# Performance work log

Measured on AMD Instinct MI355X. Metric: run time of the kernel, lower is better.

The kernel has to match this reference:

```python
import jax, jax.numpy as jnp
import numpy as np

DIM = 256
HEADS = 8
P = 8   # patch_size
S = 4   # stride


def _pos_index(p):
    # Swin-style relative position index, computed statically in numpy
    coord = np.arange(p)
    ii, jj = np.meshgrid(coord, coord, indexing='ij')
    cf = np.stack([ii.ravel(), jj.ravel()])              # [2, p*p]
    rel = cf[:, :, None] - cf[:, None, :]                # [2, P, P]
    rel = rel.transpose(1, 2, 0).copy()                  # [P, P, 2]
    rel[:, :, 0] += p - 1
    rel[:, :, 1] += p - 1
    rel[:, :, 0] *= 2 * p - 1
    return jnp.asarray(rel.sum(-1))                      # [P, P] int


def setup_inputs() -> dict:
    key = jax.random.key(0)
    k1, k2, k3, k4, k5 = jax.random.split(key, 5)
    x = jax.random.normal(k1, (2, DIM, 96, 96), jnp.float32)
    # depthwise 1x1 conv on 3*dim channels -> per-channel scale + bias
    qkv_w = jax.random.normal(k2, (3 * DIM,), jnp.float32) * 0.1 + 1.0
    qkv_b = jax.random.normal(k3, (3 * DIM,), jnp.float32) * 0.1
    # 1x1 conv dim->dim, no bias
    out_w = jax.random.normal(k4, (DIM, DIM), jnp.float32) * 0.05
    # relative position bias table, trunc_normal(std=0.02)
    pos_table = jax.random.normal(k5, ((2 * P - 1) ** 2, HEADS), jnp.float32) * 0.02
    return {"x": x, "qkv_w": qkv_w, "qkv_b": qkv_b, "out_w": out_w, "pos_table": pos_table}


def reference(x, qkv_w, qkv_b, out_w, pos_table):
    B, C, H, W = x.shape
    h, p, s = HEADS, P, S
    d = C // h
    pad = p - s
    # replicate pad right/bottom
    xp = jnp.pad(x, ((0, 0), (0, 0), (0, pad), (0, pad)), mode='edge')
    x3 = jnp.concatenate([xp, xp, xp], axis=1)           # [B, 3C, Hp, Wp]
    # depthwise 1x1 conv == per-channel affine
    qkv = x3 * qkv_w[None, :, None, None] + qkv_b[None, :, None, None]
    n = (H + pad - p) // s + 1                           # patches per side
    idx = (jnp.arange(n) * s)[:, None] + jnp.arange(p)[None, :]   # [n, p]
    # unfold: extract overlapping p x p patches with stride s
    t = qkv[:, :, idx, :]                                # [B, 3C, n, p, Wp]
    t = t[:, :, :, :, idx]                               # [B, 3C, n, p, n, p]
    t = t.transpose(0, 1, 2, 4, 3, 5)                    # [B, 3C, n, n, p, p]
    t = t.reshape(B, 3, h, d, n * n, p * p).transpose(1, 0, 2, 4, 5, 3)  # [3,B,h,N,P,d]
    q, k, v = t[0] * (d ** -0.5), t[1], t[2]
    bias = pos_table[_pos_index(p)]                      # [P, P, h]
    bias = bias.transpose(2, 0, 1)                       # [h, P, P]
    attn = jnp.einsum('bhnqd,bhnkd->bhnqk', q, k) + bias[None, :, None]
    attn = jax.nn.softmax(attn, axis=-1)
    out = jnp.einsum('bhnqk,bhnkd->bhnqd', attn, v)      # [B, h, N, P, d]
    # keep only the top-left stride x stride of each patch, then fold (non-overlap)
    out = out.reshape(B, h, n, n, p, p, d)[:, :, :, :, :s, :s]   # [B,h,n,n,s,s,d]
    out = out.transpose(0, 1, 6, 2, 4, 3, 5).reshape(B, C, H, W)
    return jnp.einsum('oc,bchw->bohw', out_w, out)
```

## Files before the change

### kernel.cpp

```cpp
#include <hip/hip_runtime.h>

typedef float f4 __attribute__((ext_vector_type(4)));
typedef float f32x4 __attribute__((ext_vector_type(4)));
typedef __bf16 bf16x8 __attribute__((ext_vector_type(8)));
typedef __bf16 bf16x4 __attribute__((ext_vector_type(4)));

#define NPSIDE 24

#define XS(ch_, r_, c_) xs[(ch_) * 169 + (r_) * 21 + (c_)]

__global__ __launch_bounds__(256, 4) void patch_attn(
    const float* __restrict__ x,
    const float* __restrict__ qkv_w,
    const float* __restrict__ qkv_b,
    const float* __restrict__ pos_table,
    const float* __restrict__ wmat,
    __bf16* __restrict__ mid,
    __bf16* __restrict__ wbf)
{
    __shared__ float xs[32 * 169];
    __shared__ __bf16 Ps[4][16][72];

    const int t = threadIdx.x;

    if (blockIdx.x < 64) {
        const int i = (blockIdx.x * 256 + t) * 4;
        const int o = i >> 8, c = i & 255;
        const f4 v = *(const f4*)&wmat[i];
        bf16x4 ov;
        #pragma unroll
        for (int j = 0; j < 4; ++j) ov[j] = (__bf16)v[j];
        *(bf16x4*)&wbf[((o >> 4) * 8 + (c >> 5)) * 512 + (o & 15) * 32 + (c & 31)] = ov;
    }

    const int raw = blockIdx.x;
    const int xcd = raw & 7;
    const int idx = raw >> 3;
    const int bs  = xcd * 36 + (idx >> 3);
    const int head = idx & 7;
    const int b   = bs / 144;
    const int r   = bs % 144;
    const int ni   = r / 6;
    const int nj0p = (r % 6) * 4;
    const int c0   = head * 32;

    #pragma unroll
    for (int i = 0; i < 5; ++i) {
        const int idx2 = i * 256 + t;
        const int ch  = idx2 / 40;
        const int rem = idx2 % 40;
        const int row = rem / 5, cg = rem % 5;
        const int rg  = min(4 * ni + row, 95);
        const int cg4 = 16 * (r % 6) + 4 * cg;
        const float* xrow = x + (((size_t)b * 256 + c0 + ch) * 96 + rg) * 96;
        f4 v;
        if (cg4 <= 92) {
            v = *(const f4*)&xrow[cg4];
        } else {
            const float s = xrow[95];
            v = (f4){s, s, s, s};
        }
        float* xdst = &XS(ch, row, 4 * cg);
        xdst[0] = v.x; xdst[1] = v.y; xdst[2] = v.z; xdst[3] = v.w;
    }

    const int wv = t >> 6, l = t & 63;
    const int l16 = l & 15, lg = l >> 4;
    const float qscale = 0.17677669529663687f;

    float kw8[8], kb8[8], qw8[8], qb8[8];
    #pragma unroll
    for (int j = 0; j < 8; ++j) {
        const int c = c0 + 8 * lg + j;
        kw8[j] = qkv_w[256 + c];
        kb8[j] = qkv_b[256 + c];
        qw8[j] = qkv_w[c] * qscale;
        qb8[j] = qkv_b[c] * qscale;
    }
    float vw2[2], vb2[2];
    #pragma unroll
    for (int nt = 0; nt < 2; ++nt) {
        const int c = c0 + nt * 16 + l16;
        vw2[nt] = qkv_w[512 + c];
        vb2[nt] = qkv_b[512 + c];
    }

    __syncthreads();

    const int nj  = nj0p + wv;
    const int cbl = 4 * wv;

    bf16x8 qf;
    {
        const int qrow = l16 >> 2, qcol = cbl + (l16 & 3);
        #pragma unroll
        for (int j = 0; j < 8; ++j)
            qf[j] = (__bf16)(XS(8 * lg + j, qrow, qcol) * qw8[j] + qb8[j]);
    }

    const f32x4 zf = {0.f, 0.f, 0.f, 0.f};
    f32x4 sacc[4];
    #pragma unroll
    for (int t4 = 0; t4 < 4; ++t4) {
        const int px = l16 + 16 * t4;
        const int kr = px >> 3, kc = cbl + (px & 7);
        bf16x8 kf;
        #pragma unroll
        for (int j = 0; j < 8; ++j)
            kf[j] = (__bf16)(XS(8 * lg + j, kr, kc) * kw8[j] + kb8[j]);
        sacc[t4] = __builtin_amdgcn_mfma_f32_16x16x32_bf16(qf, kf, zf, 0, 0, 0);
    }

    float sv[4][4], rinv[4];
    #pragma unroll
    for (int rr = 0; rr < 4; ++rr) {
        const int qrow = lg * 4 + rr;
        const int qi = qrow >> 2, qj = qrow & 3;
        float m = -1e30f;
        #pragma unroll
        for (int t4 = 0; t4 < 4; ++t4) {
            const int kcol = l16 + 16 * t4;
            const int ki = kcol >> 3, kj = kcol & 7;
            const float s = sacc[t4][rr]
                + pos_table[((qi - ki + 7) * 15 + (qj - kj + 7)) * 8 + head];
            sv[t4][rr] = s;
            m = fmaxf(m, s);
        }
        #pragma unroll
        for (int off = 8; off >= 1; off >>= 1)
            m = fmaxf(m, __shfl_xor(m, off, 16));
        float sum = 0.f;
        #pragma unroll
        for (int t4 = 0; t4 < 4; ++t4) {
            const float p = __expf(sv[t4][rr] - m);
            sv[t4][rr] = p;
            sum += p;
        }
        #pragma unroll
        for (int off = 8; off >= 1; off >>= 1)
            sum += __shfl_xor(sum, off, 16);
        rinv[rr] = 1.0f / sum;
        #pragma unroll
        for (int t4 = 0; t4 < 4; ++t4)
            Ps[wv][qrow][l16 + 16 * t4] = (__bf16)sv[t4][rr];
    }

    f32x4 oa = zf, ob = zf;
    #pragma unroll
    for (int kt = 0; kt < 2; ++kt) {
        bf16x8 pf = *(const bf16x8*)&Ps[wv][l16][lg * 8 + 32 * kt];
        bf16x8 v0, v1;
        #pragma unroll
        for (int j = 0; j < 8; ++j) {
            const int px = kt * 32 + 8 * lg + j;
            const int vr = px >> 3, vc = cbl + (px & 7);
            v0[j] = (__bf16)(XS(l16,      vr, vc) * vw2[0] + vb2[0]);
            v1[j] = (__bf16)(XS(16 + l16, vr, vc) * vw2[1] + vb2[1]);
        }
        oa = __builtin_amdgcn_mfma_f32_16x16x32_bf16(pf, v0, oa, 0, 0, 0);
        ob = __builtin_amdgcn_mfma_f32_16x16x32_bf16(pf, v1, ob, 0, 0, 0);
    }

    const int pbase = ni * 384 + lg * 96 + nj * 4;
    __bf16* mbb = mid + (size_t)b * 9216 * 256;
    #pragma unroll
    for (int rr = 0; rr < 4; ++rr) {
        const int p = pbase + rr;
        __bf16* dst = mbb + ((p >> 4) * 8 + head) * 512 + (p & 15) * 32;
        dst[l16]      = (__bf16)(oa[rr] * rinv[rr]);
        dst[16 + l16] = (__bf16)(ob[rr] * rinv[rr]);
    }
}

__global__ __launch_bounds__(256) void proj(
    const __bf16* __restrict__ wbf,
    const __bf16* __restrict__ mid,
    float* __restrict__ y)
{
    __shared__ __align__(16) __bf16 wlds[4][8][512];

    const int t  = threadIdx.x;
    const int wv = t >> 6;
    const int l  = t & 63;
    const int l16 = l & 15, lg = l >> 4;
    const int fragoff = l16 * 32 + lg * 8;

    const int raw = blockIdx.x;
    const int xcd = raw & 7;
    const int seq = raw >> 3;
    const int pair = seq >> 2;
    const int og4  = seq & 3;
    const int bs = xcd * 36 + pair;
    const int b  = bs / 144;
    const int r  = bs % 144;
    const int ni = r / 6, wcol = r % 6;
    const int ot0 = og4 * 4;
    const int pt  = (4 * ni + wv) * 6 + wcol;

    {
        const bf16x8* wsrc = (const bf16x8*)&wbf[(size_t)ot0 * 8 * 512];
        bf16x8* wdst = (bf16x8*)&wlds[0][0][0];
        #pragma unroll
        for (int i = 0; i < 8; ++i)
            wdst[t + 256 * i] = wsrc[t + 256 * i];
    }
    __syncthreads();

    const __bf16* midb = mid + ((size_t)b * 9216 + (size_t)pt * 16) * 256;
    bf16x8 bfr[8];
    #pragma unroll
    for (int kt = 0; kt < 8; ++kt)
        bfr[kt] = *(const bf16x8*)&midb[kt * 512 + fragoff];

    f32x4 acc[4];
    #pragma unroll
    for (int ot = 0; ot < 4; ++ot) acc[ot] = (f32x4){0.f, 0.f, 0.f, 0.f};

    #pragma unroll
    for (int ot = 0; ot < 4; ++ot)
        #pragma unroll
        for (int kt = 0; kt < 8; ++kt) {
            const bf16x8 af = *(const bf16x8*)&wlds[ot][kt][fragoff];
            acc[ot] = __builtin_amdgcn_mfma_f32_16x16x32_bf16(af, bfr[kt], acc[ot], 0, 0, 0);
        }

    const int p = pt * 16 + l16;
    #pragma unroll
    for (int ot = 0; ot < 4; ++ot) {
        const int o = (ot0 + ot) * 16 + lg * 4;
        float* yb = y + ((size_t)b * 256 + o) * 9216 + p;
        #pragma unroll
        for (int rr = 0; rr < 4; ++rr)
            yb[(size_t)rr * 9216] = acc[ot][rr];
    }
}

extern "C" void kernel_launch(void* const* d_in, const int* in_sizes, int n_in,
                              void* d_out, int out_size, void* d_ws, size_t ws_size,
                              hipStream_t stream) {
    const float* x         = (const float*)d_in[0];
    const float* qkv_w     = (const float*)d_in[1];
    const float* qkv_b     = (const float*)d_in[2];
    const float* out_w     = (const float*)d_in[3];
    const float* pos_table = (const float*)d_in[4];
    float* y    = (float*)d_out;
    __bf16* mid = (__bf16*)d_ws;
    __bf16* wbf = (__bf16*)((char*)d_ws + (12u << 20));

    patch_attn<<<dim3(2304), dim3(256), 0, stream>>>(
        x, qkv_w, qkv_b, pos_table, out_w, mid, wbf);
    proj<<<dim3(1152), dim3(256), 0, stream>>>(
        wbf, mid, y);
}
```

Baseline: 33.27 us.

## Precompute Q/K/V in bf16 shared-memory layouts matching MFMA fragments

Replaces the fp32 raw-input shared tile with separate bf16 K, Q and V tiles. The per-channel affine and bf16 conversion are applied once at load time, and each tile is stored in the layout the MFMA operands read. This removes the repeated affine math and the scattered scalar LDS reads when building fragments, since K and Q fragments become single 16-byte loads. In exchange, global loads shrink to float2 per channel with strided channel access, and only 320 of 512 thread slots do load work.

```diff
diff --git a/kernel.cpp b/kernel.cpp
--- a/kernel.cpp
+++ b/kernel.cpp
@@ -1,13 +1,13 @@
 #include <hip/hip_runtime.h>
 
 typedef float f4 __attribute__((ext_vector_type(4)));
+typedef float f2 __attribute__((ext_vector_type(2)));
 typedef float f32x4 __attribute__((ext_vector_type(4)));
 typedef __bf16 bf16x8 __attribute__((ext_vector_type(8)));
 typedef __bf16 bf16x4 __attribute__((ext_vector_type(4)));
+typedef __bf16 bf16x2 __attribute__((ext_vector_type(2)));
 
 #define NPSIDE 24
-
-#define XS(ch_, r_, c_) xs[(ch_) * 169 + (r_) * 21 + (c_)]
 
 __global__ __launch_bounds__(256, 4) void patch_attn(
     const float* __restrict__ x,
@@ -18,7 +18,9 @@
     __bf16* __restrict__ mid,
     __bf16* __restrict__ wbf)
 {
-    __shared__ float xs[32 * 169];
+    __shared__ __bf16 Kreg[160][40];
+    __shared__ __bf16 Qreg[4][16][40];
+    __shared__ __bf16 Vreg[32][196];
     __shared__ __bf16 Ps[4][16][72];
 
     const int t = threadIdx.x;
@@ -43,71 +45,78 @@
     const int ni   = r / 6;
     const int nj0p = (r % 6) * 4;
     const int c0   = head * 32;
-
-    #pragma unroll
-    for (int i = 0; i < 5; ++i) {
-        const int idx2 = i * 256 + t;
-        const int ch  = idx2 / 40;
-        const int rem = idx2 % 40;
-        const int row = rem / 5, cg = rem % 5;
-        const int rg  = min(4 * ni + row, 95);
-        const int cg4 = 16 * (r % 6) + 4 * cg;
-        const float* xrow = x + (((size_t)b * 256 + c0 + ch) * 96 + rg) * 96;
-        f4 v;
-        if (cg4 <= 92) {
-            v = *(const f4*)&xrow[cg4];
-        } else {
-            const float s = xrow[95];
-            v = (f4){s, s, s, s};
-        }
-        float* xdst = &XS(ch, row, 4 * cg);
-        xdst[0] = v.x; xdst[1] = v.y; xdst[2] = v.z; xdst[3] = v.w;
-    }
+    const float qscale = 0.17677669529663687f;
+
+    #pragma unroll
+    for (int pass = 0; pass < 2; ++pass) {
+        const int u = pass * 256 + t;
+        if (u < 320) {
+            const int chg = u / 80;
+            const int rem = u % 80;
+            const int row = rem / 10, cp = rem % 10;
+            const int col0 = 2 * cp;
+            const int rg = min(4 * ni + row, 95);
+            const int cg = 16 * (r % 6) + col0;
+            const int cb8 = c0 + 8 * chg;
+            const float* xb = x + (((size_t)b * 256 + cb8) * 96 + rg) * 96;
+            const f4 kw0 = *(const f4*)&qkv_w[256 + cb8], kw1 = *(const f4*)&qkv_w[260 + cb8];
+            const f4 kb0 = *(const f4*)&qkv_b[256 + cb8], kb1 = *(const f4*)&qkv_b[260 + cb8];
+            const f4 vw0 = *(const f4*)&qkv_w[512 + cb8], vw1 = *(const f4*)&qkv_w[516 + cb8];
+            const f4 vb0 = *(const f4*)&qkv_b[512 + cb8], vb1 = *(const f4*)&qkv_b[516 + cb8];
+            const f4 qw0 = *(const f4*)&qkv_w[cb8],       qw1 = *(const f4*)&qkv_w[cb8 + 4];
+            const f4 qb0 = *(const f4*)&qkv_b[cb8],       qb1 = *(const f4*)&qkv_b[cb8 + 4];
+            const bool own = (row < 4) && (col0 < 16);
+            bf16x8 k0v, k1v, q0v, q1v;
+            #pragma unroll
+            for (int j = 0; j < 8; ++j) {
+                const float kw = j < 4 ? kw0[j] : kw1[j - 4];
+                const float kb = j < 4 ? kb0[j] : kb1[j - 4];
+                const float vw = j < 4 ? vw0[j] : vw1[j - 4];
+                const float vb = j < 4 ? vb0[j] : vb1[j - 4];
+                const float qw = (j < 4 ? qw0[j] : qw1[j - 4]) * qscale;
+                const float qb = (j < 4 ? qb0[j] : qb1[j - 4]) * qscale;
+                f2 xv;
+                if (cg <= 94) {
+                    xv = *(const f2*)&xb[(size_t)j * 9216 + cg];
+                } else {
+                    const float s = xb[(size_t)j * 9216 + 95];
+                    xv.x = s; xv.y = s;
+                }
+                k0v[j] = (__bf16)(xv.x * kw + kb);
+                k1v[j] = (__bf16)(xv.y * kw + kb);
+                bf16x2 vv;
+                vv[0] = (__bf16)(xv.x * vw + vb);
+                vv[1] = (__bf16)(xv.y * vw + vb);
+                *(bf16x2*)&Vreg[8 * chg + j][row * 24 + col0] = vv;
+                q0v[j] = (__bf16)(xv.x * qw + qb);
+                q1v[j] = (__bf16)(xv.y * qw + qb);
+            }
+            const int px0 = row * 20 + col0;
+            *(bf16x8*)&Kreg[px0][8 * chg]     = k0v;
+            *(bf16x8*)&Kreg[px0 + 1][8 * chg] = k1v;
+            if (own) {
+                const int wvp = col0 >> 2;
+                const int q0 = (row << 2) | (col0 & 3);
+                *(bf16x8*)&Qreg[wvp][q0][8 * chg]     = q0v;
+                *(bf16x8*)&Qreg[wvp][q0 + 1][8 * chg] = q1v;
+            }
+        }
+    }
+    __syncthreads();
 
     const int wv = t >> 6, l = t & 63;
     const int l16 = l & 15, lg = l >> 4;
-    const float qscale = 0.17677669529663687f;
-
-    float kw8[8], kb8[8], qw8[8], qb8[8];
-    #pragma unroll
-    for (int j = 0; j < 8; ++j) {
-        const int c = c0 + 8 * lg + j;
-        kw8[j] = qkv_w[256 + c];
-        kb8[j] = qkv_b[256 + c];
-        qw8[j] = qkv_w[c] * qscale;
-        qb8[j] = qkv_b[c] * qscale;
-    }
-    float vw2[2], vb2[2];
-    #pragma unroll
-    for (int nt = 0; nt < 2; ++nt) {
-        const int c = c0 + nt * 16 + l16;
-        vw2[nt] = qkv_w[512 + c];
-        vb2[nt] = qkv_b[512 + c];
-    }
-
-    __syncthreads();
-
-    const int nj  = nj0p + wv;
-    const int cbl = 4 * wv;
-
-    bf16x8 qf;
-    {
-        const int qrow = l16 >> 2, qcol = cbl + (l16 & 3);
-        #pragma unroll
-        for (int j = 0; j < 8; ++j)
-            qf[j] = (__bf16)(XS(8 * lg + j, qrow, qcol) * qw8[j] + qb8[j]);
-    }
+    const int nj = nj0p + wv;
+    const int cw = 4 * wv;
 
     const f32x4 zf = {0.f, 0.f, 0.f, 0.f};
+    const bf16x8 qf = *(const bf16x8*)&Qreg[wv][l16][lg * 8];
     f32x4 sacc[4];
     #pragma unroll
     for (int t4 = 0; t4 < 4; ++t4) {
         const int px = l16 + 16 * t4;
-        const int kr = px >> 3, kc = cbl + (px & 7);
-        bf16x8 kf;
-        #pragma unroll
-        for (int j = 0; j < 8; ++j)
-            kf[j] = (__bf16)(XS(8 * lg + j, kr, kc) * kw8[j] + kb8[j]);
+        const bf16x8 kf =
+            *(const bf16x8*)&Kreg[(px >> 3) * 20 + cw + (px & 7)][lg * 8];
         sacc[t4] = __builtin_amdgcn_mfma_f32_16x16x32_bf16(qf, kf, zf, 0, 0, 0);
     }
 
@@ -148,14 +157,17 @@
     f32x4 oa = zf, ob = zf;
     #pragma unroll
     for (int kt = 0; kt < 2; ++kt) {
-        bf16x8 pf = *(const bf16x8*)&Ps[wv][l16][lg * 8 + 32 * kt];
+        const bf16x8 pf = *(const bf16x8*)&Ps[wv][l16][lg * 8 + 32 * kt];
+        const int pos = (4 * kt + lg) * 24 + cw;
+        const bf16x4 a0 = *(const bf16x4*)&Vreg[l16][pos];
+        const bf16x4 a1 = *(const bf16x4*)&Vreg[l16][pos + 4];
+        const bf16x4 b0 = *(const bf16x4*)&Vreg[16 + l16][pos];
+        const bf16x4 b1 = *(const bf16x4*)&Vreg[16 + l16][pos + 4];
         bf16x8 v0, v1;
         #pragma unroll
-        for (int j = 0; j < 8; ++j) {
-            const int px = kt * 32 + 8 * lg + j;
-            const int vr = px >> 3, vc = cbl + (px & 7);
-            v0[j] = (__bf16)(XS(l16,      vr, vc) * vw2[0] + vb2[0]);
-            v1[j] = (__bf16)(XS(16 + l16, vr, vc) * vw2[1] + vb2[1]);
+        for (int j = 0; j < 4; ++j) {
+            v0[j] = a0[j]; v0[4 + j] = a1[j];
+            v1[j] = b0[j]; v1[4 + j] = b1[j];
         }
         oa = __builtin_amdgcn_mfma_f32_16x16x32_bf16(pf, v0, oa, 0, 0, 0);
         ob = __builtin_amdgcn_mfma_f32_16x16x32_bf16(pf, v1, ob, 0, 0, 0);
```

Measured after the change: 42.25 us. +27.0%, slower.
